# Optimization experiments

Measured on AMD Instinct MI355X. Metric: run time of the kernel, lower is better.

Reference implementation:

```python
import jax, jax.numpy as jnp
import numpy as np

PARAMETER = 0.1
INPUT_SIZE = 512
OUTPUT_SIZE = 512


def setup_inputs() -> dict:
    key = jax.random.key(0)
    k1, k2, k3 = jax.random.split(key, 3)
    T, B = 4096, 32
    input_tensor = jax.random.normal(k1, (T, B, INPUT_SIZE), dtype=jnp.float32)
    k = np.sqrt(1.0 / INPUT_SIZE)
    weight = jax.random.uniform(k2, (OUTPUT_SIZE, INPUT_SIZE), dtype=jnp.float32, minval=-k, maxval=k)
    bias = jax.random.uniform(k3, (OUTPUT_SIZE,), dtype=jnp.float32, minval=-k, maxval=k)
    return {"input_tensor": input_tensor, "weight": weight, "bias": bias}


def reference(input_tensor, weight, bias):
    # linear projection: [T, B, I] @ [I, O] -> [T, B, O]
    y = jnp.einsum('tbi,oi->tbo', input_tensor, weight) + bias

    # EMA recurrence: v[0] = y[0]; v[t] = p * v[t-1] + y[t]
    def step(carry, yt):
        v = PARAMETER * carry + yt
        return v, v

    _, rest = jax.lax.scan(step, y[0], y[1:])
    return jnp.concatenate([y[:1], rest], axis=0)
```

## Files before the change

kernel.cpp:

```cpp
#include <hip/hip_runtime.h>
#include <hip/hip_bf16.h>

#define T_DIM 4096
#define B_DIM 32
#define I_DIM 512
#define O_DIM 512
#define M_DIM (T_DIM * B_DIM)
#define PARAM 0.1f
#define ISCALE 1.1111112f

#define STRIP 64
#define TAPS 8

#define BM 128
#define BN 256
#define BK 64
#define NK (I_DIM / BK)

typedef __attribute__((ext_vector_type(8))) short bf16x8;
typedef __attribute__((ext_vector_type(4))) float f32x4;

__device__ __forceinline__ unsigned short f2bf(float f) {
    union { __hip_bfloat16 b; unsigned short u; } cv;
    cv.b = __float2bfloat16(f);
    return cv.u;
}

__global__ __launch_bounds__(256) void wcvt_kernel(const float* __restrict__ W,
                                                   unsigned short* __restrict__ Wb) {
    const int i = (blockIdx.x * 256 + threadIdx.x) * 4;
    f32x4 v = *(const f32x4*)(W + i);
    ushort4 o;
    o.x = f2bf(v[0]); o.y = f2bf(v[1]); o.z = f2bf(v[2]); o.w = f2bf(v[3]);
    *(ushort4*)(Wb + i) = o;
}

__global__ __launch_bounds__(256) void xema_kernel(const float* __restrict__ X,
                                                   unsigned short* __restrict__ Xv) {
    const int s   = blockIdx.x >> 4;
    const int blk = blockIdx.x & 15;
    const int col = (blk * 256 + threadIdx.x) * 4;
    const int t0  = s * STRIP;
    const int b   = col >> 9;
    const int o   = col & 511;

    const float* xin = X + (size_t)t0 * 16384 + col;
    unsigned short* xout = Xv + (size_t)(t0 * 32 + b) * 512 + o;

    f32x4 v = {0.f, 0.f, 0.f, 0.f};
    if (s > 0) {
        const float* w = xin - (size_t)TAPS * 16384;
        #pragma unroll
        for (int j = 0; j < TAPS; ++j)
            v = PARAM * v + *(const f32x4*)(w + (size_t)j * 16384);
    }

    f32x4 bufA[8], bufB[8];
    #pragma unroll
    for (int j = 0; j < 8; ++j) bufA[j] = *(const f32x4*)(xin + (size_t)j * 16384);

    #pragma unroll
    for (int i = 0; i < STRIP; i += 16) {
        #pragma unroll
        for (int j = 0; j < 8; ++j)
            bufB[j] = *(const f32x4*)(xin + (size_t)(i + 8 + j) * 16384);
        #pragma unroll
        for (int j = 0; j < 8; ++j) {
            v = PARAM * v + bufA[j];
            ushort4 pk; pk.x = f2bf(v[0]); pk.y = f2bf(v[1]); pk.z = f2bf(v[2]); pk.w = f2bf(v[3]);
            *(ushort4*)(xout + (size_t)(i + j) * 16384) = pk;
        }
        if (i + 16 < STRIP) {
            #pragma unroll
            for (int j = 0; j < 8; ++j)
                bufA[j] = *(const f32x4*)(xin + (size_t)(i + 16 + j) * 16384);
        }
        #pragma unroll
        for (int j = 0; j < 8; ++j) {
            v = PARAM * v + bufB[j];
            ushort4 pk; pk.x = f2bf(v[0]); pk.y = f2bf(v[1]); pk.z = f2bf(v[2]); pk.w = f2bf(v[3]);
            *(ushort4*)(xout + (size_t)(i + 8 + j) * 16384) = pk;
        }
    }
}

__global__ __launch_bounds__(512, 2) void gemm_kernel(const unsigned short* __restrict__ Xv,
                                                      const unsigned short* __restrict__ Wb,
                                                      const float* __restrict__ bias,
                                                      float* __restrict__ Y) {
    __shared__ __align__(16) short As[3][BM * BK];
    __shared__ __align__(16) short Bs[3][BN * BK];

    const int tid  = threadIdx.x;
    const int lane = tid & 63;
    const int wave = tid >> 6;
    const int wm   = wave >> 2;
    const int wn   = wave & 3;

    const int bid = blockIdx.x;
    const int j   = bid >> 3;
    const int bn  = j & 1;
    const int mt  = (bid & 7) * 128 + (j >> 1);
    const int row0 = mt * BM;
    const int col0 = bn * BN;

    const int cs = (tid & 7) ^ ((tid >> 3) & 7);
    const unsigned short* aSrc = Xv + (size_t)(row0 + (tid >> 3)) * 512 + cs * 8;
    const unsigned short* bSrc = Wb + (size_t)(col0 + (tid >> 3)) * 512 + cs * 8;

    #define STAGE(buf, k0)                                                            \
        do {                                                                          \
            _Pragma("unroll")                                                         \
            for (int it_ = 0; it_ < 2; ++it_)                                         \
                __builtin_amdgcn_global_load_lds(                                     \
                    (const __attribute__((address_space(1))) unsigned int*)(aSrc + (size_t)it_ * 64 * 512 + (k0)), \
                    (__attribute__((address_space(3))) unsigned int*)(&As[buf][0] + (it_ * 512 + wave * 64) * 8),  \
                    16, 0, 0);                                                        \
            _Pragma("unroll")                                                         \
            for (int it_ = 0; it_ < 4; ++it_)                                         \
                __builtin_amdgcn_global_load_lds(                                     \
                    (const __attribute__((address_space(1))) unsigned int*)(bSrc + (size_t)it_ * 64 * 512 + (k0)), \
                    (__attribute__((address_space(3))) unsigned int*)(&Bs[buf][0] + (it_ * 512 + wave * 64) * 8),  \
                    16, 0, 0);                                                        \
        } while (0)

    f32x4 acc[4][4] = {};

    #define COMPUTE(buf)                                                              \
        do {                                                                          \
            _Pragma("unroll")                                                         \
            for (int kk = 0; kk < 2; ++kk) {                                          \
                const int cc = kk * 4 + (lane >> 4);                                  \
                bf16x8 a_[4], b_[4];                                                  \
                _Pragma("unroll")                                                     \
                for (int mf = 0; mf < 4; ++mf) {                                      \
                    const int r = wm * 64 + mf * 16 + (lane & 15);                    \
                    a_[mf] = *(const bf16x8*)((const char*)&As[buf][0] + r * 128 + ((cc ^ (r & 7)) << 4)); \
                }                                                                     \
                _Pragma("unroll")                                                     \
                for (int nf = 0; nf < 4; ++nf) {                                      \
                    const int r = wn * 64 + nf * 16 + (lane & 15);                    \
                    b_[nf] = *(const bf16x8*)((const char*)&Bs[buf][0] + r * 128 + ((cc ^ (r & 7)) << 4)); \
                }                                                                     \
                __builtin_amdgcn_s_setprio(1);                                        \
                _Pragma("unroll")                                                     \
                for (int mf = 0; mf < 4; ++mf)                                        \
                    _Pragma("unroll")                                                 \
                    for (int nf = 0; nf < 4; ++nf)                                    \
                        acc[mf][nf] = __builtin_amdgcn_mfma_f32_16x16x32_bf16(        \
                            a_[mf], b_[nf], acc[mf][nf], 0, 0, 0);                    \
                __builtin_amdgcn_s_setprio(0);                                        \
            }                                                                         \
        } while (0)

    #define KITER(k, vm, buf)                                                         \
        do {                                                                          \
            asm volatile("s_waitcnt vmcnt(" #vm ")" ::: "memory");                    \
            __builtin_amdgcn_sched_barrier(0);                                        \
            __builtin_amdgcn_s_barrier();                                             \
            asm volatile("" ::: "memory");                                            \
            COMPUTE(buf);                                                             \
            asm volatile("" ::: "memory");                                            \
            __builtin_amdgcn_s_barrier();                                             \
            asm volatile("" ::: "memory");                                            \
            if ((k) + 3 < NK) STAGE(buf, ((k) + 3) * BK);                             \
        } while (0)

    STAGE(0, 0 * BK);
    STAGE(1, 1 * BK);
    STAGE(2, 2 * BK);

    KITER(0, 12, 0);
    KITER(1, 12, 1);
    KITER(2, 12, 2);
    KITER(3, 12, 0);
    KITER(4, 12, 1);
    KITER(5, 12, 2);
    KITER(6,  6, 0);
    KITER(7,  0, 1);

    float sc[4][4];
    #pragma unroll
    for (int mf = 0; mf < 4; ++mf)
        #pragma unroll
        for (int jj = 0; jj < 4; ++jj) {
            const int t = (row0 + wm * 64 + mf * 16 + ((lane >> 4) << 2) + jj) >> 5;
            sc[mf][jj] = (1.0f - __expf(-2.3025851f * (float)(t + 1))) * ISCALE;
        }

    #pragma unroll
    for (int mf = 0; mf < 4; ++mf) {
        #pragma unroll
        for (int nf = 0; nf < 4; ++nf) {
            const int gcol = col0 + wn * 64 + nf * 16 + (lane & 15);
            const float bv = bias[gcol];
            #pragma unroll
            for (int jj = 0; jj < 4; ++jj) {
                const int grow = row0 + wm * 64 + mf * 16 + ((lane >> 4) << 2) + jj;
                Y[(size_t)grow * O_DIM + gcol] = acc[mf][nf][jj] + sc[mf][jj] * bv;
            }
        }
    }
}

extern "C" void kernel_launch(void* const* d_in, const int* in_sizes, int n_in,
                              void* d_out, int out_size, void* d_ws, size_t ws_size,
                              hipStream_t stream) {
    const float* X    = (const float*)d_in[0];
    const float* W    = (const float*)d_in[1];
    const float* bias = (const float*)d_in[2];
    float* Y = (float*)d_out;
    unsigned short* Wb = (unsigned short*)d_ws;
    unsigned short* Xv = (unsigned short*)((char*)d_ws + (1 << 20));

    wcvt_kernel<<<dim3(O_DIM * I_DIM / (256 * 4)), dim3(256), 0, stream>>>(W, Wb);
    xema_kernel<<<dim3((T_DIM / STRIP) * 16), dim3(256), 0, stream>>>(X, Xv);
    gemm_kernel<<<dim3((M_DIM / BM) * (O_DIM / BN)), dim3(512), 0, stream>>>(Xv, Wb, bias, Y);
}
```

Before: 240.5 us.

## Enlarge GEMM tile to 256x256 with double-buffered quadrant-phased MFMA schedule

Doubles the GEMM M tile to 256 rows, so each wave accumulates 128x64 outputs. The pipeline drops from three buffers to two, and each K tile is split into four quadrant phases that interleave LDS fragment reads with MFMA, with barriers between phases. It also halves the EMA strip length so the prefilter kernel launches more blocks, and it simplifies the epilogue's scale and bias loads. The larger tile raises reuse per LDS byte but increases register pressure, adds more barriers, and reduces the number of GEMM blocks in flight.

After: 240.5 us. No clear change (+0.0%).

```diff
diff --git a/kernel.cpp b/kernel.cpp
--- a/kernel.cpp
+++ b/kernel.cpp
@@ -9,10 +9,10 @@
 #define PARAM 0.1f
 #define ISCALE 1.1111112f
 
-#define STRIP 64
+#define STRIP 32
 #define TAPS 8
 
-#define BM 128
+#define BM 256
 #define BN 256
 #define BK 64
 #define NK (I_DIM / BK)
@@ -55,31 +55,31 @@
             v = PARAM * v + *(const f32x4*)(w + (size_t)j * 16384);
     }
 
-    f32x4 bufA[8], bufB[8];
-    #pragma unroll
-    for (int j = 0; j < 8; ++j) bufA[j] = *(const f32x4*)(xin + (size_t)j * 16384);
-
-    #pragma unroll
-    for (int i = 0; i < STRIP; i += 16) {
-        #pragma unroll
-        for (int j = 0; j < 8; ++j)
-            bufB[j] = *(const f32x4*)(xin + (size_t)(i + 8 + j) * 16384);
-        #pragma unroll
-        for (int j = 0; j < 8; ++j) {
+    f32x4 bufA[4], bufB[4];
+    #pragma unroll
+    for (int j = 0; j < 4; ++j) bufA[j] = *(const f32x4*)(xin + (size_t)j * 16384);
+
+    #pragma unroll
+    for (int i = 0; i < STRIP; i += 8) {
+        #pragma unroll
+        for (int j = 0; j < 4; ++j)
+            bufB[j] = *(const f32x4*)(xin + (size_t)(i + 4 + j) * 16384);
+        #pragma unroll
+        for (int j = 0; j < 4; ++j) {
             v = PARAM * v + bufA[j];
             ushort4 pk; pk.x = f2bf(v[0]); pk.y = f2bf(v[1]); pk.z = f2bf(v[2]); pk.w = f2bf(v[3]);
             *(ushort4*)(xout + (size_t)(i + j) * 16384) = pk;
         }
-        if (i + 16 < STRIP) {
+        if (i + 8 < STRIP) {
             #pragma unroll
-            for (int j = 0; j < 8; ++j)
-                bufA[j] = *(const f32x4*)(xin + (size_t)(i + 16 + j) * 16384);
-        }
-        #pragma unroll
-        for (int j = 0; j < 8; ++j) {
+            for (int j = 0; j < 4; ++j)
+                bufA[j] = *(const f32x4*)(xin + (size_t)(i + 8 + j) * 16384);
+        }
+        #pragma unroll
+        for (int j = 0; j < 4; ++j) {
             v = PARAM * v + bufB[j];
             ushort4 pk; pk.x = f2bf(v[0]); pk.y = f2bf(v[1]); pk.z = f2bf(v[2]); pk.w = f2bf(v[3]);
-            *(ushort4*)(xout + (size_t)(i + 8 + j) * 16384) = pk;
+            *(ushort4*)(xout + (size_t)(i + 4 + j) * 16384) = pk;
         }
     }
 }
@@ -88,8 +88,8 @@
                                                       const unsigned short* __restrict__ Wb,
                                                       const float* __restrict__ bias,
                                                       float* __restrict__ Y) {
-    __shared__ __align__(16) short As[3][BM * BK];
-    __shared__ __align__(16) short Bs[3][BN * BK];
+    __shared__ __align__(16) short As[2][BM * BK];
+    __shared__ __align__(16) short Bs[2][BN * BK];
 
     const int tid  = threadIdx.x;
     const int lane = tid & 63;
@@ -97,10 +97,10 @@
     const int wm   = wave >> 2;
     const int wn   = wave & 3;
 
-    const int bid = blockIdx.x;
-    const int j   = bid >> 3;
-    const int bn  = j & 1;
-    const int mt  = (bid & 7) * 128 + (j >> 1);
+    const int bid  = blockIdx.x;
+    const int swz  = (bid & 7) * 128 + (bid >> 3);
+    const int bn   = swz & 1;
+    const int mt   = swz >> 1;
     const int row0 = mt * BM;
     const int col0 = bn * BN;
 
@@ -108,96 +108,124 @@
     const unsigned short* aSrc = Xv + (size_t)(row0 + (tid >> 3)) * 512 + cs * 8;
     const unsigned short* bSrc = Wb + (size_t)(col0 + (tid >> 3)) * 512 + cs * 8;
 
-    #define STAGE(buf, k0)                                                            \
-        do {                                                                          \
-            _Pragma("unroll")                                                         \
-            for (int it_ = 0; it_ < 2; ++it_)                                         \
+    #define STAGE_TILE(d, kt)                                                         \
+        do {                                                                          \
+            _Pragma("unroll")                                                         \
+            for (int s_ = 0; s_ < 4; ++s_)                                            \
                 __builtin_amdgcn_global_load_lds(                                     \
-                    (const __attribute__((address_space(1))) unsigned int*)(aSrc + (size_t)it_ * 64 * 512 + (k0)), \
-                    (__attribute__((address_space(3))) unsigned int*)(&As[buf][0] + (it_ * 512 + wave * 64) * 8),  \
+                    (const __attribute__((address_space(1))) unsigned int*)(aSrc + (size_t)s_ * 64 * 512 + (kt) * 64), \
+                    (__attribute__((address_space(3))) unsigned int*)(&As[d][0] + (s_ * 512 + tid) * 8),              \
                     16, 0, 0);                                                        \
             _Pragma("unroll")                                                         \
-            for (int it_ = 0; it_ < 4; ++it_)                                         \
+            for (int s_ = 0; s_ < 4; ++s_)                                            \
                 __builtin_amdgcn_global_load_lds(                                     \
-                    (const __attribute__((address_space(1))) unsigned int*)(bSrc + (size_t)it_ * 64 * 512 + (k0)), \
-                    (__attribute__((address_space(3))) unsigned int*)(&Bs[buf][0] + (it_ * 512 + wave * 64) * 8),  \
+                    (const __attribute__((address_space(1))) unsigned int*)(bSrc + (size_t)s_ * 64 * 512 + (kt) * 64), \
+                    (__attribute__((address_space(3))) unsigned int*)(&Bs[d][0] + (s_ * 512 + tid) * 8),              \
                     16, 0, 0);                                                        \
         } while (0)
 
-    f32x4 acc[4][4] = {};
-
-    #define COMPUTE(buf)                                                              \
-        do {                                                                          \
-            _Pragma("unroll")                                                         \
-            for (int kk = 0; kk < 2; ++kk) {                                          \
-                const int cc = kk * 4 + (lane >> 4);                                  \
-                bf16x8 a_[4], b_[4];                                                  \
+    f32x4 acc[8][4] = {};
+    bf16x8 af[4][2];
+    bf16x8 bf2[2][2];
+
+    #define READ_A(d, rg)                                                             \
+        do {                                                                          \
+            _Pragma("unroll")                                                         \
+            for (int m_ = 0; m_ < 4; ++m_)                                            \
                 _Pragma("unroll")                                                     \
-                for (int mf = 0; mf < 4; ++mf) {                                      \
-                    const int r = wm * 64 + mf * 16 + (lane & 15);                    \
-                    a_[mf] = *(const bf16x8*)((const char*)&As[buf][0] + r * 128 + ((cc ^ (r & 7)) << 4)); \
+                for (int kk_ = 0; kk_ < 2; ++kk_) {                                   \
+                    const int r_  = wm * 128 + (rg) * 64 + m_ * 16 + (lane & 15);     \
+                    const int cc_ = kk_ * 4 + (lane >> 4);                            \
+                    af[m_][kk_] = *(const bf16x8*)((const char*)&As[d][0] + r_ * 128 + ((cc_ ^ (r_ & 7)) << 4)); \
                 }                                                                     \
+        } while (0)
+
+    #define READ_B(d, cg)                                                             \
+        do {                                                                          \
+            _Pragma("unroll")                                                         \
+            for (int n_ = 0; n_ < 2; ++n_)                                            \
                 _Pragma("unroll")                                                     \
-                for (int nf = 0; nf < 4; ++nf) {                                      \
-                    const int r = wn * 64 + nf * 16 + (lane & 15);                    \
-                    b_[nf] = *(const bf16x8*)((const char*)&Bs[buf][0] + r * 128 + ((cc ^ (r & 7)) << 4)); \
+                for (int kk_ = 0; kk_ < 2; ++kk_) {                                   \
+                    const int r_  = wn * 64 + (cg) * 32 + n_ * 16 + (lane & 15);      \
+                    const int cc_ = kk_ * 4 + (lane >> 4);                            \
+                    bf2[n_][kk_] = *(const bf16x8*)((const char*)&Bs[d][0] + r_ * 128 + ((cc_ ^ (r_ & 7)) << 4)); \
                 }                                                                     \
-                __builtin_amdgcn_s_setprio(1);                                        \
+        } while (0)
+
+    #define MFMA_Q(rg, cg)                                                            \
+        do {                                                                          \
+            __builtin_amdgcn_s_setprio(1);                                            \
+            _Pragma("unroll")                                                         \
+            for (int kk_ = 0; kk_ < 2; ++kk_)                                         \
                 _Pragma("unroll")                                                     \
-                for (int mf = 0; mf < 4; ++mf)                                        \
+                for (int m_ = 0; m_ < 4; ++m_)                                        \
                     _Pragma("unroll")                                                 \
-                    for (int nf = 0; nf < 4; ++nf)                                    \
-                        acc[mf][nf] = __builtin_amdgcn_mfma_f32_16x16x32_bf16(        \
-                            a_[mf], b_[nf], acc[mf][nf], 0, 0, 0);                    \
-                __builtin_amdgcn_s_setprio(0);                                        \
-            }                                                                         \
-        } while (0)
-
-    #define KITER(k, vm, buf)                                                         \
-        do {                                                                          \
-            asm volatile("s_waitcnt vmcnt(" #vm ")" ::: "memory");                    \
+                    for (int n_ = 0; n_ < 2; ++n_)                                    \
+                        acc[(rg) * 4 + m_][(cg) * 2 + n_] =                           \
+                            __builtin_amdgcn_mfma_f32_16x16x32_bf16(                  \
+                                af[m_][kk_], bf2[n_][kk_],                            \
+                                acc[(rg) * 4 + m_][(cg) * 2 + n_], 0, 0, 0);          \
+            __builtin_amdgcn_s_setprio(0);                                            \
+        } while (0)
+
+    #define PHASE_SYNC()                                                              \
+        do {                                                                          \
+            __builtin_amdgcn_s_barrier();                                             \
+            asm volatile("s_waitcnt lgkmcnt(0)" ::: "memory");                        \
             __builtin_amdgcn_sched_barrier(0);                                        \
-            __builtin_amdgcn_s_barrier();                                             \
-            asm volatile("" ::: "memory");                                            \
-            COMPUTE(buf);                                                             \
-            asm volatile("" ::: "memory");                                            \
-            __builtin_amdgcn_s_barrier();                                             \
-            asm volatile("" ::: "memory");                                            \
-            if ((k) + 3 < NK) STAGE(buf, ((k) + 3) * BK);                             \
-        } while (0)
-
-    STAGE(0, 0 * BK);
-    STAGE(1, 1 * BK);
-    STAGE(2, 2 * BK);
-
-    KITER(0, 12, 0);
-    KITER(1, 12, 1);
-    KITER(2, 12, 2);
-    KITER(3, 12, 0);
-    KITER(4, 12, 1);
-    KITER(5, 12, 2);
-    KITER(6,  6, 0);
-    KITER(7,  0, 1);
-
-    float sc[4][4];
-    #pragma unroll
-    for (int mf = 0; mf < 4; ++mf)
-        #pragma unroll
-        for (int jj = 0; jj < 4; ++jj) {
-            const int t = (row0 + wm * 64 + mf * 16 + ((lane >> 4) << 2) + jj) >> 5;
-            sc[mf][jj] = (1.0f - __expf(-2.3025851f * (float)(t + 1))) * ISCALE;
-        }
-
-    #pragma unroll
-    for (int mf = 0; mf < 4; ++mf) {
+        } while (0)
+
+    #define TILE(t, DOSTAGE)                                                          \
+        do {                                                                          \
+            READ_A((t) & 1, 0); READ_B((t) & 1, 0);                                   \
+            if (DOSTAGE) STAGE_TILE(((t) & 1) ^ 1, (t) + 1);                          \
+            PHASE_SYNC(); MFMA_Q(0, 0);                                               \
+            __builtin_amdgcn_s_barrier();                                             \
+            READ_B((t) & 1, 1);                                                       \
+            PHASE_SYNC(); MFMA_Q(0, 1);                                               \
+            __builtin_amdgcn_s_barrier();                                             \
+            READ_A((t) & 1, 1);                                                       \
+            PHASE_SYNC(); MFMA_Q(1, 1);                                               \
+            __builtin_amdgcn_s_barrier();                                             \
+            READ_B((t) & 1, 0);                                                       \
+            PHASE_SYNC(); MFMA_Q(1, 0);                                               \
+            if (DOSTAGE) asm volatile("s_waitcnt vmcnt(0)" ::: "memory");             \
+            __builtin_amdgcn_s_barrier();                                             \
+        } while (0)
+
+    STAGE_TILE(0, 0);
+    asm volatile("s_waitcnt vmcnt(0)" ::: "memory");
+    __builtin_amdgcn_s_barrier();
+
+    TILE(0, 1);
+    TILE(1, 1);
+    TILE(2, 1);
+    TILE(3, 1);
+    TILE(4, 1);
+    TILE(5, 1);
+    TILE(6, 1);
+    TILE(7, 0);
+
+    float sc4[4];
+    #pragma unroll
+    for (int tt = 0; tt < 4; ++tt) {
+        const int t_ = ((row0 + wm * 128) >> 5) + tt;
+        sc4[tt] = (1.0f - __expf(-2.3025851f * (float)(t_ + 1))) * ISCALE;
+    }
+    float bv[4];
+    #pragma unroll
+    for (int nf = 0; nf < 4; ++nf)
+        bv[nf] = bias[col0 + wn * 64 + nf * 16 + (lane & 15)];
+
+    #pragma unroll
+    for (int mf = 0; mf < 8; ++mf) {
         #pragma unroll
         for (int nf = 0; nf < 4; ++nf) {
             const int gcol = col0 + wn * 64 + nf * 16 + (lane & 15);
-            const float bv = bias[gcol];
             #pragma unroll
-            for (int jj = 0; jj < 4; ++jj) {
-                const int grow = row0 + wm * 64 + mf * 16 + ((lane >> 4) << 2) + jj;
-                Y[(size_t)grow * O_DIM + gcol] = acc[mf][nf][jj] + sc[mf][jj] * bv;
+            for (int j = 0; j < 4; ++j) {
+                const int grow = row0 + wm * 128 + mf * 16 + ((lane >> 4) << 2) + j;
+                Y[(size_t)grow * O_DIM + gcol] = acc[mf][nf][j] + sc4[mf >> 1] * bv[nf];
             }
         }
     }
```
